# Optimization experiments

Measured on AMD Instinct MI355X. Metric: run time of the kernel, lower is better.

## Reference

```python
import jax, jax.numpy as jnp
import numpy as np

ALPHA = 1.0

def setup_inputs() -> dict:
    key = jax.random.key(0)
    k1, k2 = jax.random.split(key)
    N, K, D = 524288, 256, 256
    context = jax.random.normal(k1, (N, D), dtype=jnp.float32)
    clusters = jax.random.normal(k2, (K, D), dtype=jnp.float32)
    return {"context": context, "clusters": clusters}

def reference(context, clusters):
    # Squared euclidean distance via the matmul trick: same math as
    # sum((x[:,None]-c)**2, -1) but avoids materializing (N,K,D).
    x2 = jnp.sum(context * context, axis=1, keepdims=True)          # (N,1)
    c2 = jnp.sum(clusters * clusters, axis=1)                       # (K,)
    xc = context @ clusters.T                                       # (N,K)
    distance = x2 + c2 - 2.0 * xc                                   # (N,K)
    q = 1.0 / (1.0 + distance / ALPHA)
    q = q ** ((ALPHA + 1.0) / 2.0)
    q = q / jnp.sum(q, axis=1, keepdims=True)                        # row-normalize
    return q
```

## Files before the change

kernel.cpp:

```cpp
#include <hip/hip_runtime.h>
#include <hip/hip_bf16.h>


#define DD 256
#define KC 256
#define BM 64
#define CL_SHORTS (KC * DD)

typedef __attribute__((ext_vector_type(4)))  float f32x4;
typedef __attribute__((ext_vector_type(16))) float f32x16;
typedef __attribute__((ext_vector_type(8)))  short bf16x8;
typedef __attribute__((ext_vector_type(4)))  short bf16x4;
typedef __attribute__((ext_vector_type(4)))  unsigned u32x4;

__device__ __forceinline__ short f2bf(float f) {
    union { float f; unsigned u; } v; v.f = f;
    unsigned r = (v.u + 0x7fffu + ((v.u >> 16) & 1u)) >> 16;
    return (short)r;
}

__device__ __forceinline__ unsigned cvtpk(float a, float b) {
    unsigned r;
    asm("v_cvt_pk_bf16_f32 %0, %1, %2" : "=v"(r) : "v"(a), "v"(b));
    return r;
}

__device__ __forceinline__ float frcp(float x) {
    return __builtin_amdgcn_rcpf(x);
}

template<int CTRL>
__device__ __forceinline__ float dpp_add(float v) {
    int iv = __builtin_bit_cast(int, v);
    int mv = __builtin_amdgcn_update_dpp(0, iv, CTRL, 0xf, 0xf, false);
    return v + __builtin_bit_cast(float, mv);
}
#define ROW_SHR1   0x111
#define ROW_SHR2   0x112
#define ROW_SHR4   0x114
#define ROW_SHR8   0x118
#define ROW_BC15   0x142
#define QUAD_SWAP1 0xB1

__device__ __forceinline__ float readlane_f(float v, int l) {
    return __builtin_bit_cast(float,
        __builtin_amdgcn_readlane(__builtin_bit_cast(int, v), l));
}

__device__ __forceinline__ f32x4 ld4(const float* p) { return *(const f32x4*)p; }

__global__ __launch_bounds__(64)
void prep_clusters(const float* __restrict__ clus,
                   short* __restrict__ wsb, float* __restrict__ c2) {
    const int c = blockIdx.x;
    const int t = threadIdx.x;
    f32x4 v = *(const f32x4*)(clus + c * DD + t * 4);
    bf16x4 o;
    o[0] = f2bf(v[0]); o[1] = f2bf(v[1]); o[2] = f2bf(v[2]); o[3] = f2bf(v[3]);

    const int j    = t >> 1;
    const int ks   = j >> 1;
    const int hi   = j & 1;
    const int half = t & 1;
    const int nj   = c >> 5;
    const int l31  = c & 31;
    *(bf16x4*)&wsb[(((nj * 16 + ks) * 64 + hi * 32 + l31) << 3) + half * 4] = o;

    float s = v[0]*v[0] + v[1]*v[1] + v[2]*v[2] + v[3]*v[3];
    s += __shfl_xor(s, 1);  s += __shfl_xor(s, 2);  s += __shfl_xor(s, 4);
    s += __shfl_xor(s, 8);  s += __shfl_xor(s, 16); s += __shfl_xor(s, 32);
    if (t == 0) c2[c] = s;
}

__global__ __launch_bounds__(512, 6)
void cluster_q_main(const float* __restrict__ ctx,
                    const short* __restrict__ wsb,
                    const float* __restrict__ c2g,
                    float* __restrict__ out) {
    __shared__ short Af[32 * 64 * 8];
    __shared__ float x2p8[8][BM];
    __shared__ float rowsum[8][BM];

    const int t    = threadIdx.x;
    const int lane = t & 63;
    const int w    = t >> 6;
    const int l31  = lane & 31;
    const int hi   = lane >> 5;
    const size_t row0 = (size_t)blockIdx.x * BM;

    {
        const int r0   = lane >> 1;
        const int half = lane & 1;
        f32x4 u[8];
#pragma unroll
        for (int m = 0; m < 2; ++m) {
            const float* src = ctx + (row0 + (size_t)(m * 32 + r0)) * DD
                             + w * 32 + half * 16;
#pragma unroll
            for (int i = 0; i < 4; ++i)
                u[m * 4 + i] = ld4(src + i * 4);
        }
#pragma unroll
        for (int m = 0; m < 2; ++m) {
            float xs = 0.f;
#pragma unroll
            for (int c = 0; c < 2; ++c) {
                f32x4 a0 = u[m * 4 + 2 * c], a1 = u[m * 4 + 2 * c + 1];
                u32x4 o;
                o[0] = cvtpk(a0[0], a0[1]);
                o[1] = cvtpk(a0[2], a0[3]);
                o[2] = cvtpk(a1[0], a1[1]);
                o[3] = cvtpk(a1[2], a1[3]);
                xs += a0[0]*a0[0] + a0[1]*a0[1] + a0[2]*a0[2] + a0[3]*a0[3]
                    + a1[0]*a1[0] + a1[1]*a1[1] + a1[2]*a1[2] + a1[3]*a1[3];
                const int j = w * 4 + half * 2 + c;
                *(u32x4*)&Af[(j * 64 + m * 32 + r0) * 8] = o;
            }
            xs = dpp_add<QUAD_SWAP1>(xs);
            if (half == 0) x2p8[w][m * 32 + r0] = xs;
        }
    }

    const short* bl = wsb + (size_t)(w * 16) * 512 + lane * 8;

    const float c2v = c2g[w * 32 + l31];

    __syncthreads();

    float x2A = 0.f, x2B = 0.f;
#pragma unroll
    for (int q = 0; q < 8; ++q) {
        x2A += x2p8[q][l31];
        x2B += x2p8[q][32 + l31];
    }

    f32x16 acc0 = (f32x16)0.f, acc1 = (f32x16)0.f;

    bf16x8 bs[3];
    bs[0] = *(const bf16x8*)(bl + 0 * 512);
    bs[1] = *(const bf16x8*)(bl + 1 * 512);

    bf16x8 afA0 = *(const bf16x8*)&Af[((0 + hi) * 64 +  0 + l31) * 8];
    bf16x8 afA1 = *(const bf16x8*)&Af[((0 + hi) * 64 + 32 + l31) * 8];
    bf16x8 afB0, afB1;

#pragma unroll
    for (int ks = 0; ks < 16; ++ks) {
        const int cur = ks % 3;
        const bool even = (ks & 1) == 0;

        if (ks < 14) {
            const int nxt = (ks + 2) % 3;
            bs[nxt] = *(const bf16x8*)(bl + (ks + 2) * 512);
        }
        if (ks < 15) {
            const int jn = (ks + 1) * 2 + hi;
            bf16x8 v0 = *(const bf16x8*)&Af[(jn * 64 +  0 + l31) * 8];
            bf16x8 v1 = *(const bf16x8*)&Af[(jn * 64 + 32 + l31) * 8];
            if (even) { afB0 = v0; afB1 = v1; }
            else      { afA0 = v0; afA1 = v1; }
        }

        const bf16x8 a0 = even ? afA0 : afB0;
        const bf16x8 a1 = even ? afA1 : afB1;
        acc0 = __builtin_amdgcn_mfma_f32_32x32x16_bf16(a0, bs[cur], acc0, 0, 0, 0);
        acc1 = __builtin_amdgcn_mfma_f32_32x32x16_bf16(a1, bs[cur], acc1, 0, 0, 0);
    }

#pragma unroll
    for (int r = 0; r < 16; ++r) {
        const int rr0 = (r & 3) + 8 * (r >> 2);
        {
            const float xa = readlane_f(x2A, rr0);
            const float xb = readlane_f(x2A, rr0 + 4);
            const float x2r = hi ? xb : xa;
            const float d = x2r + c2v - 2.f * acc0[r];
            float s = frcp(1.f + d);
            acc0[r] = s;
            s = dpp_add<ROW_SHR1>(s);
            s = dpp_add<ROW_SHR2>(s);
            s = dpp_add<ROW_SHR4>(s);
            s = dpp_add<ROW_SHR8>(s);
            s = dpp_add<ROW_BC15>(s);
            if (l31 == 31) rowsum[w][rr0 + 4 * hi] = s;
        }
        {
            const float xa = readlane_f(x2B, rr0);
            const float xb = readlane_f(x2B, rr0 + 4);
            const float x2r = hi ? xb : xa;
            const float d = x2r + c2v - 2.f * acc1[r];
            float s = frcp(1.f + d);
            acc1[r] = s;
            s = dpp_add<ROW_SHR1>(s);
            s = dpp_add<ROW_SHR2>(s);
            s = dpp_add<ROW_SHR4>(s);
            s = dpp_add<ROW_SHR8>(s);
            s = dpp_add<ROW_BC15>(s);
            if (l31 == 31) rowsum[w][32 + rr0 + 4 * hi] = s;
        }
    }
    __syncthreads();

    float slA = 0.f, slB = 0.f;
#pragma unroll
    for (int q = 0; q < 8; ++q) {
        slA += rowsum[q][l31];
        slB += rowsum[q][32 + l31];
    }
    const float invA = frcp(slA);
    const float invB = frcp(slB);

#pragma unroll
    for (int r = 0; r < 16; ++r) {
        const int rr0 = (r & 3) + 8 * (r >> 2);
        {
            const float ia = readlane_f(invA, rr0);
            const float ib = readlane_f(invA, rr0 + 4);
            const float inv = hi ? ib : ia;
            float* op = out + (row0 + (size_t)(rr0 + 4 * hi)) * KC + w * 32 + l31;
            op[0] = acc0[r] * inv;
        }
        {
            const float ia = readlane_f(invB, rr0);
            const float ib = readlane_f(invB, rr0 + 4);
            const float inv = hi ? ib : ia;
            float* op = out + (row0 + (size_t)(32 + rr0 + 4 * hi)) * KC + w * 32 + l31;
            op[0] = acc1[r] * inv;
        }
    }
}

extern "C" void kernel_launch(void* const* d_in, const int* in_sizes, int n_in,
                              void* d_out, int out_size, void* d_ws, size_t ws_size,
                              hipStream_t stream) {
    const float* ctx  = (const float*)d_in[0];
    const float* clus = (const float*)d_in[1];
    float* out = (float*)d_out;

    short* wsb = (short*)d_ws;
    float* c2  = (float*)((char*)d_ws + CL_SHORTS * 2);

    const int nrows = in_sizes[0] / DD;
    const int grid  = nrows / BM;

    hipLaunchKernelGGL(prep_clusters, dim3(KC), dim3(64), 0, stream, clus, wsb, c2);
    hipLaunchKernelGGL(cluster_q_main, dim3(grid), dim3(512), 0, stream,
                       ctx, wsb, c2, out);
}
```

Before: 246.8 us.

## Fold distance bias terms into an extra MFMA step and vectorize output stores

Scales the cluster operand by -2 and adds a 17th K-step whose A/B fragments carry x2 and 1+c2 as triple-bf16 splits against ones. The MFMA accumulator then directly yields 1+distance, which removes the per-element readlane/bias epilogue. Swapping the MFMA operand order transposes the accumulator layout, so each lane holds whole rows. Row sums become plain per-lane adds instead of DPP reductions, and outputs go out as float4 stores. The cost is one extra MFMA pair, an extra barrier and LDS slot, and possible precision loss from the bf16-split bias terms.

```diff
diff --git a/kernel.cpp b/kernel.cpp
--- a/kernel.cpp
+++ b/kernel.cpp
@@ -5,7 +5,6 @@
 #define DD 256
 #define KC 256
 #define BM 64
-#define CL_SHORTS (KC * DD)
 
 typedef __attribute__((ext_vector_type(4)))  float f32x4;
 typedef __attribute__((ext_vector_type(16))) float f32x16;
@@ -19,6 +18,10 @@
     return (short)r;
 }
 
+__device__ __forceinline__ float bf2f(short h) {
+    return __builtin_bit_cast(float, ((unsigned)(unsigned short)h) << 16);
+}
+
 __device__ __forceinline__ unsigned cvtpk(float a, float b) {
     unsigned r;
     asm("v_cvt_pk_bf16_f32 %0, %1, %2" : "=v"(r) : "v"(a), "v"(b));
@@ -35,28 +38,18 @@
     int mv = __builtin_amdgcn_update_dpp(0, iv, CTRL, 0xf, 0xf, false);
     return v + __builtin_bit_cast(float, mv);
 }
-#define ROW_SHR1   0x111
-#define ROW_SHR2   0x112
-#define ROW_SHR4   0x114
-#define ROW_SHR8   0x118
-#define ROW_BC15   0x142
 #define QUAD_SWAP1 0xB1
 
-__device__ __forceinline__ float readlane_f(float v, int l) {
-    return __builtin_bit_cast(float,
-        __builtin_amdgcn_readlane(__builtin_bit_cast(int, v), l));
-}
-
 __device__ __forceinline__ f32x4 ld4(const float* p) { return *(const f32x4*)p; }
 
 __global__ __launch_bounds__(64)
-void prep_clusters(const float* __restrict__ clus,
-                   short* __restrict__ wsb, float* __restrict__ c2) {
+void prep_clusters(const float* __restrict__ clus, short* __restrict__ wsb) {
     const int c = blockIdx.x;
     const int t = threadIdx.x;
     f32x4 v = *(const f32x4*)(clus + c * DD + t * 4);
     bf16x4 o;
-    o[0] = f2bf(v[0]); o[1] = f2bf(v[1]); o[2] = f2bf(v[2]); o[3] = f2bf(v[3]);
+    o[0] = f2bf(-2.f * v[0]); o[1] = f2bf(-2.f * v[1]);
+    o[2] = f2bf(-2.f * v[2]); o[3] = f2bf(-2.f * v[3]);
 
     const int j    = t >> 1;
     const int ks   = j >> 1;
@@ -64,22 +57,35 @@
     const int half = t & 1;
     const int nj   = c >> 5;
     const int l31  = c & 31;
-    *(bf16x4*)&wsb[(((nj * 16 + ks) * 64 + hi * 32 + l31) << 3) + half * 4] = o;
+    *(bf16x4*)&wsb[(((nj * 17 + ks) * 64 + hi * 32 + l31) << 3) + half * 4] = o;
 
     float s = v[0]*v[0] + v[1]*v[1] + v[2]*v[2] + v[3]*v[3];
     s += __shfl_xor(s, 1);  s += __shfl_xor(s, 2);  s += __shfl_xor(s, 4);
     s += __shfl_xor(s, 8);  s += __shfl_xor(s, 16); s += __shfl_xor(s, 32);
-    if (t == 0) c2[c] = s;
+    if (t == 0) {
+        float e = 1.f + s;
+        short h = f2bf(e);  float e1 = e - bf2f(h);
+        short m = f2bf(e1); float e2 = e1 - bf2f(m);
+        short l = f2bf(e2);
+        const unsigned one = 0x3F80u;
+        u32x4 a;
+        a[0] = one | (one << 16);
+        a[1] = one | ((unsigned)(unsigned short)h << 16);
+        a[2] = (unsigned)(unsigned short)m | ((unsigned)(unsigned short)l << 16);
+        a[3] = 0u;
+        *(u32x4*)&wsb[((nj * 17 + 16) * 64 + l31) * 8] = a;
+        u32x4 z = {0u, 0u, 0u, 0u};
+        *(u32x4*)&wsb[((nj * 17 + 16) * 64 + 32 + l31) * 8] = z;
+    }
 }
 
 __global__ __launch_bounds__(512, 6)
 void cluster_q_main(const float* __restrict__ ctx,
                     const short* __restrict__ wsb,
-                    const float* __restrict__ c2g,
                     float* __restrict__ out) {
-    __shared__ short Af[32 * 64 * 8];
-    __shared__ float x2p8[8][BM];
-    __shared__ float rowsum[8][BM];
+    __shared__ short Af[34 * 64 * 8];
+    __shared__ float x2p8[8][64];
+    __shared__ float rowsum2[8][2][64];
 
     const int t    = threadIdx.x;
     const int lane = t & 63;
@@ -121,17 +127,26 @@
         }
     }
 
-    const short* bl = wsb + (size_t)(w * 16) * 512 + lane * 8;
-
-    const float c2v = c2g[w * 32 + l31];
+    const short* bl = wsb + (size_t)(w * 17) * 512 + lane * 8;
 
     __syncthreads();
 
-    float x2A = 0.f, x2B = 0.f;
-#pragma unroll
-    for (int q = 0; q < 8; ++q) {
-        x2A += x2p8[q][l31];
-        x2B += x2p8[q][32 + l31];
+    if (w == 0) {
+        float e = 0.f;
+#pragma unroll
+        for (int q = 0; q < 8; ++q) e += x2p8[q][lane];
+        short h = f2bf(e);  float e1 = e - bf2f(h);
+        short m = f2bf(e1); float e2 = e1 - bf2f(m);
+        short l = f2bf(e2);
+        const unsigned one = 0x3F80u;
+        u32x4 o;
+        o[0] = (unsigned)(unsigned short)h | ((unsigned)(unsigned short)m << 16);
+        o[1] = (unsigned)(unsigned short)l | (one << 16);
+        o[2] = one | (one << 16);
+        o[3] = 0u;
+        *(u32x4*)&Af[(32 * 64 + lane) * 8] = o;
+        u32x4 z = {0u, 0u, 0u, 0u};
+        *(u32x4*)&Af[(33 * 64 + lane) * 8] = z;
     }
 
     f32x16 acc0 = (f32x16)0.f, acc1 = (f32x16)0.f;
@@ -149,10 +164,8 @@
         const int cur = ks % 3;
         const bool even = (ks & 1) == 0;
 
-        if (ks < 14) {
-            const int nxt = (ks + 2) % 3;
-            bs[nxt] = *(const bf16x8*)(bl + (ks + 2) * 512);
-        }
+        if (ks < 14)
+            bs[(ks + 2) % 3] = *(const bf16x8*)(bl + (ks + 2) * 512);
         if (ks < 15) {
             const int jn = (ks + 1) * 2 + hi;
             bf16x8 v0 = *(const bf16x8*)&Af[(jn * 64 +  0 + l31) * 8];
@@ -163,70 +176,52 @@
 
         const bf16x8 a0 = even ? afA0 : afB0;
         const bf16x8 a1 = even ? afA1 : afB1;
-        acc0 = __builtin_amdgcn_mfma_f32_32x32x16_bf16(a0, bs[cur], acc0, 0, 0, 0);
-        acc1 = __builtin_amdgcn_mfma_f32_32x32x16_bf16(a1, bs[cur], acc1, 0, 0, 0);
-    }
-
+        acc0 = __builtin_amdgcn_mfma_f32_32x32x16_bf16(bs[cur], a0, acc0, 0, 0, 0);
+        acc1 = __builtin_amdgcn_mfma_f32_32x32x16_bf16(bs[cur], a1, acc1, 0, 0, 0);
+    }
+
+    bf16x8 bsa = *(const bf16x8*)(bl + 16 * 512);
+
+    __syncthreads();
+
+    {
+        bf16x8 aa0 = *(const bf16x8*)&Af[((32 + hi) * 64 +  0 + l31) * 8];
+        bf16x8 aa1 = *(const bf16x8*)&Af[((32 + hi) * 64 + 32 + l31) * 8];
+        acc0 = __builtin_amdgcn_mfma_f32_32x32x16_bf16(bsa, aa0, acc0, 0, 0, 0);
+        acc1 = __builtin_amdgcn_mfma_f32_32x32x16_bf16(bsa, aa1, acc1, 0, 0, 0);
+    }
+
+    float s0 = 0.f, s1 = 0.f;
 #pragma unroll
     for (int r = 0; r < 16; ++r) {
-        const int rr0 = (r & 3) + 8 * (r >> 2);
-        {
-            const float xa = readlane_f(x2A, rr0);
-            const float xb = readlane_f(x2A, rr0 + 4);
-            const float x2r = hi ? xb : xa;
-            const float d = x2r + c2v - 2.f * acc0[r];
-            float s = frcp(1.f + d);
-            acc0[r] = s;
-            s = dpp_add<ROW_SHR1>(s);
-            s = dpp_add<ROW_SHR2>(s);
-            s = dpp_add<ROW_SHR4>(s);
-            s = dpp_add<ROW_SHR8>(s);
-            s = dpp_add<ROW_BC15>(s);
-            if (l31 == 31) rowsum[w][rr0 + 4 * hi] = s;
-        }
-        {
-            const float xa = readlane_f(x2B, rr0);
-            const float xb = readlane_f(x2B, rr0 + 4);
-            const float x2r = hi ? xb : xa;
-            const float d = x2r + c2v - 2.f * acc1[r];
-            float s = frcp(1.f + d);
-            acc1[r] = s;
-            s = dpp_add<ROW_SHR1>(s);
-            s = dpp_add<ROW_SHR2>(s);
-            s = dpp_add<ROW_SHR4>(s);
-            s = dpp_add<ROW_SHR8>(s);
-            s = dpp_add<ROW_BC15>(s);
-            if (l31 == 31) rowsum[w][32 + rr0 + 4 * hi] = s;
-        }
-    }
+        acc0[r] = frcp(acc0[r]); s0 += acc0[r];
+        acc1[r] = frcp(acc1[r]); s1 += acc1[r];
+    }
+    rowsum2[w][hi][l31]      = s0;
+    rowsum2[w][hi][32 + l31] = s1;
     __syncthreads();
 
-    float slA = 0.f, slB = 0.f;
+    float t0 = 0.f, t1 = 0.f;
 #pragma unroll
     for (int q = 0; q < 8; ++q) {
-        slA += rowsum[q][l31];
-        slB += rowsum[q][32 + l31];
-    }
-    const float invA = frcp(slA);
-    const float invB = frcp(slB);
-
-#pragma unroll
-    for (int r = 0; r < 16; ++r) {
-        const int rr0 = (r & 3) + 8 * (r >> 2);
-        {
-            const float ia = readlane_f(invA, rr0);
-            const float ib = readlane_f(invA, rr0 + 4);
-            const float inv = hi ? ib : ia;
-            float* op = out + (row0 + (size_t)(rr0 + 4 * hi)) * KC + w * 32 + l31;
-            op[0] = acc0[r] * inv;
-        }
-        {
-            const float ia = readlane_f(invB, rr0);
-            const float ib = readlane_f(invB, rr0 + 4);
-            const float inv = hi ? ib : ia;
-            float* op = out + (row0 + (size_t)(32 + rr0 + 4 * hi)) * KC + w * 32 + l31;
-            op[0] = acc1[r] * inv;
-        }
+        t0 += rowsum2[q][0][l31]      + rowsum2[q][1][l31];
+        t1 += rowsum2[q][0][32 + l31] + rowsum2[q][1][32 + l31];
+    }
+    const float inv0 = frcp(t0);
+    const float inv1 = frcp(t1);
+
+    float* op0 = out + (row0 + (size_t)l31) * KC        + w * 32 + 4 * hi;
+    float* op1 = out + (row0 + (size_t)(32 + l31)) * KC + w * 32 + 4 * hi;
+#pragma unroll
+    for (int i = 0; i < 4; ++i) {
+        f32x4 v0, v1;
+#pragma unroll
+        for (int j = 0; j < 4; ++j) {
+            v0[j] = acc0[4 * i + j] * inv0;
+            v1[j] = acc1[4 * i + j] * inv1;
+        }
+        *(f32x4*)(op0 + 8 * i) = v0;
+        *(f32x4*)(op1 + 8 * i) = v1;
     }
 }
 
@@ -238,12 +233,11 @@
     float* out = (float*)d_out;
 
     short* wsb = (short*)d_ws;
-    float* c2  = (float*)((char*)d_ws + CL_SHORTS * 2);
 
     const int nrows = in_sizes[0] / DD;
     const int grid  = nrows / BM;
 
-    hipLaunchKernelGGL(prep_clusters, dim3(KC), dim3(64), 0, stream, clus, wsb, c2);
+    hipLaunchKernelGGL(prep_clusters, dim3(KC), dim3(64), 0, stream, clus, wsb);
     hipLaunchKernelGGL(cluster_q_main, dim3(grid), dim3(512), 0, stream,
-                       ctx, wsb, c2, out);
-}
+                       ctx, wsb, out);
+}
```

Result: faster. 240.9 us (median of 2 runs) (-2.4%).
